# Performance work log

Hardware: AMD Instinct MI355X
Metric: run time of the kernel (lower is better)

## Reference

```python
import jax, jax.numpy as jnp
import numpy as np

N, F, H, K, E = 10000, 128, 128, 500, 320000
EPS = 1e-15


def setup_inputs() -> dict:
    key = jax.random.key(0)
    ks = jax.random.split(key, 16)
    def lin(k, fi, fo):
        return jax.random.normal(k, (fi, fo), jnp.float32) / np.sqrt(fi).astype(np.float32)
    inp = {
        'nodes': jax.random.normal(ks[0], (N, F), jnp.float32),
        'edges': jax.random.randint(ks[1], (2, E), 0, N, jnp.int32),
        'batch': jnp.zeros((N,), jnp.int32),
        'W1': lin(ks[2], F, H), 'b1': jnp.zeros((H,), jnp.float32),
        'W2': lin(ks[3], H, H), 'b2': jnp.zeros((H,), jnp.float32),
        'pool_W': lin(ks[4], H, K), 'pool_b': jnp.zeros((K,), jnp.float32),
        'W3': lin(ks[5], H, H), 'b3': jnp.zeros((H,), jnp.float32),
        'W4': lin(ks[6], H, H), 'b4': jnp.zeros((H,), jnp.float32),
        'W5': lin(ks[7], H, F), 'b5': jnp.zeros((F,), jnp.float32),
    }
    return inp


def reference(nodes, edges, batch, W1, b1, W2, b2, pool_W, pool_b, W3, b3, W4, b4, W5, b5):
    n = nodes.shape[0]
    row, col = edges[0], edges[1]
    # GCN normalization with self-loops (computed once, shared by all convs)
    loop = jnp.arange(n, dtype=row.dtype)
    row_sl = jnp.concatenate([row, loop])
    col_sl = jnp.concatenate([col, loop])
    deg = jax.ops.segment_sum(jnp.ones_like(col_sl, dtype=nodes.dtype), col_sl, num_segments=n)
    dinv = jnp.where(deg > 0, 1.0 / jnp.sqrt(deg), 0.0)
    norm = dinv[row_sl] * dinv[col_sl]  # [E+N]

    def gcn(x, W, b):
        h = x @ W
        msg = h[row_sl] * norm[:, None]
        return jax.ops.segment_sum(msg, col_sl, num_segments=n) + b

    x = jnp.tanh(gcn(nodes, W1, b1))
    x = jnp.tanh(gcn(x, W2, b2))

    # dense batch (single graph) + dense adjacency [1, N, N]
    adj = jnp.zeros((n, n), x.dtype).at[row, col].add(1.0)[None]
    xd = x[None]                                   # [1, N, H]
    s_logits = xd @ pool_W + pool_b                # [1, N, K]

    # ---- dense_mincut_pool ----
    s = jax.nn.softmax(s_logits, axis=-1)
    k = s.shape[-1]
    out = jnp.einsum('bnk,bnh->bkh', s, xd)        # s^T x, [1, K, H]
    a_s = adj @ s                                  # [1, N, K]
    out_adj = jnp.swapaxes(s, 1, 2) @ a_s          # s^T A s, [1, K, K]
    mincut_num = jnp.trace(out_adj, axis1=1, axis2=2)
    d_flat = adj.sum(-1)                           # [1, N]
    # trace(s^T D s) = sum_n d_n * sum_k s_nk^2
    mincut_den = jnp.einsum('bn,bnk,bnk->b', d_flat, s, s) + EPS
    mincut_loss = jnp.mean(-(mincut_num / mincut_den))
    ss = jnp.swapaxes(s, 1, 2) @ s                 # [1, K, K]
    ss_norm = jnp.linalg.norm(ss, axis=(-1, -2), keepdims=True)
    i_s_normed = jnp.eye(k, dtype=ss.dtype) / jnp.sqrt(jnp.asarray(k, ss.dtype))
    ortho_loss = jnp.mean(jnp.linalg.norm(ss / (ss_norm + EPS) - i_s_normed, axis=(-1, -2)))
    # zero diagonal, then symmetric degree normalization
    out_adj = out_adj * (1.0 - jnp.eye(k, dtype=out_adj.dtype))
    d = jnp.sqrt(out_adj.sum(-1))[:, None] + EPS   # [1, 1, K]
    out_adj = out_adj / d / jnp.swapaxes(d, 1, 2)
    # ---- end pool ----

    s2 = jax.nn.softmax(s_logits, axis=-1)
    x_out = (s2 @ out)[0]                          # [N, H]
    adj_out = s2 @ (out_adj @ jnp.swapaxes(s2, 1, 2))  # [1, N, N]

    # recon_adj = False -> reuse original edge_index
    x = jnp.tanh(gcn(x_out, W3, b3))
    x = jnp.tanh(gcn(x, W4, b4))
    x = gcn(x, W5, b5)
    return x, adj_out, mincut_loss, ortho_loss
```

## Files before the change

### kernel.cpp

```cpp
#include <hip/hip_runtime.h>
#include <hip/hip_bf16.h>
#include <math.h>

#define EPSF 1e-15f

typedef __attribute__((ext_vector_type(8))) short bf16x8;
typedef __attribute__((ext_vector_type(4))) float f32x4;

__device__ __forceinline__ void gload_lds16(const void* g, void* l){
  __builtin_amdgcn_global_load_lds(
    (const __attribute__((address_space(1))) unsigned int*)(g),
    (__attribute__((address_space(3))) unsigned int*)(l), 16, 0, 0);
}


__global__ void k_count_deg(const int* __restrict__ edges, int E, int* indeg, int* outdeg){
  int e = blockIdx.x*blockDim.x + threadIdx.x;
  if (e >= E) return;
  int r = edges[e], c = edges[E+e];
  atomicAdd(&outdeg[r], 1);
  atomicAdd(&indeg[c], 1);
}

__global__ void k_scan_fused(const int* __restrict__ cnt, int* __restrict__ rowptr,
                             int* __restrict__ cur, float* __restrict__ dinvOut, int n){
  __shared__ int csum[257];
  const int T = 256;
  int chunk = (n + T - 1)/T;
  int t = threadIdx.x;
  int beg = t*chunk, end = min(n, beg + chunk);
  int s = 0;
  for (int i = beg; i < end; ++i) s += cnt[i];
  csum[t+1] = s;
  if (t == 0) csum[0] = 0;
  __syncthreads();
  if (t == 0){ for (int i = 1; i <= T; ++i) csum[i] += csum[i-1]; }
  __syncthreads();
  int acc = csum[t];
  for (int i = beg; i < end; ++i){
    rowptr[i] = acc;
    cur[i] = acc;
    if (dinvOut) dinvOut[i] = rsqrtf((float)(cnt[i] + 1));
    acc += cnt[i];
  }
  if (t == T-1) rowptr[n] = csum[T];
}

__global__ void k_fill_csr(const int* __restrict__ edges, int E, int* cur_in, int* cur_out,
                           int* __restrict__ src, int* __restrict__ dst){
  int e = blockIdx.x*blockDim.x + threadIdx.x;
  if (e >= E) return;
  int r = edges[e], c = edges[E+e];
  int p = atomicAdd(&cur_in[c], 1);  src[p] = r;
  int q = atomicAdd(&cur_out[r], 1); dst[q] = c;
}

__global__ __launch_bounds__(128)
void k_gcn_agg_b(const __hip_bfloat16* __restrict__ hb, const float* __restrict__ dinv,
                 const int* __restrict__ rowptr, const int* __restrict__ src,
                 const float* __restrict__ bias, float* __restrict__ outf,
                 __hip_bfloat16* __restrict__ outb, int Hd, int do_tanh){
  int c = blockIdx.x;
  int t = threadIdx.x;
  float dc = dinv[c];
  float sum = __bfloat162float(hb[(size_t)c*Hd + t]) * dc;
  float sum2 = 0.f;
  int e0 = rowptr[c], e1 = rowptr[c+1];
  int e = e0;
  for (; e + 1 < e1; e += 2){
    int sa = src[e], sb2 = src[e+1];
    sum  += __bfloat162float(hb[(size_t)sa*Hd  + t]) * dinv[sa];
    sum2 += __bfloat162float(hb[(size_t)sb2*Hd + t]) * dinv[sb2];
  }
  if (e < e1){
    int sa = src[e];
    sum += __bfloat162float(hb[(size_t)sa*Hd + t]) * dinv[sa];
  }
  sum += sum2;
  float v = sum * dc + bias[t];
  if (do_tanh) v = tanhf(v);
  if (outf) outf[(size_t)c*Hd + t] = v;
  if (outb) outb[(size_t)c*Hd + t] = __float2bfloat16(v);
}

__global__ __launch_bounds__(256)
void k_as_agg_b2(const __hip_bfloat16* __restrict__ sb, const int* __restrict__ rowptr,
                 const int* __restrict__ dst, float* __restrict__ a_s, int K2, int KP2){
  int n = blockIdx.x;
  int e0 = rowptr[n], e1 = rowptr[n+1];
  const unsigned* sb32 = (const unsigned*)sb;
  for (int k = threadIdx.x; k < K2; k += blockDim.x){
    float a0 = 0.f, a1 = 0.f;
    for (int e = e0; e < e1; ++e){
      unsigned v = sb32[(size_t)dst[e]*KP2 + k];
      a0 += __uint_as_float(v << 16);
      a1 += __uint_as_float(v & 0xFFFF0000u);
    }
    float2* o = (float2*)(a_s + (size_t)n*(K2*2));
    o[k] = make_float2(a0, a1);
  }
}

__global__ void k_pack_bf16pad(const float* __restrict__ x, __hip_bfloat16* __restrict__ y,
                               int rows, int K, int KP){
  long long n = (long long)rows*KP;
  for (long long i = (long long)blockIdx.x*blockDim.x + threadIdx.x; i < n;
       i += (long long)gridDim.x*blockDim.x){
    int row = (int)(i / KP), col = (int)(i - (long long)row*KP);
    y[i] = (col < K) ? __float2bfloat16(x[(size_t)row*K + col]) : __float2bfloat16(0.f);
  }
}

__device__ __forceinline__ void transpose_tile(const float* X, __hip_bfloat16* XT,
                                               int R, int C, int Cp, int Np,
                                               int bx, int by){
  __shared__ float t[32][33];
  int jb = bx*32;
  int ib = by*32;
  int tx = threadIdx.x & 31, ty = threadIdx.x >> 5;
  #pragma unroll
  for (int k = 0; k < 4; ++k){
    int i = ib + ty + k*8, j = jb + tx;
    t[ty + k*8][tx] = (i < R && j < C) ? X[(size_t)i*C + j] : 0.f;
  }
  __syncthreads();
  #pragma unroll
  for (int k = 0; k < 4; ++k){
    int jr = jb + ty + k*8, ic = ib + tx;
    if (jr < Cp && ic < Np)
      XT[(size_t)jr*Np + ic] = __float2bfloat16(t[tx][ty + k*8]);
  }
}

__global__ __launch_bounds__(256)
void k_transpose_f2b(const float* __restrict__ X, __hip_bfloat16* __restrict__ XT,
                     int R, int C, int Cp, int Np){
  transpose_tile(X, XT, R, C, Cp, Np, blockIdx.x, blockIdx.y);
}

struct TPar { const float* src; __hip_bfloat16* dst; int R, C, Cp, Np; };

__global__ __launch_bounds__(256)
void k_transpose_batch6(TPar p0, TPar p1, TPar p2, TPar p3, TPar p4, TPar p5){
  TPar p;
  switch (blockIdx.z){
    case 0: p = p0; break;
    case 1: p = p1; break;
    case 2: p = p2; break;
    case 3: p = p3; break;
    case 4: p = p4; break;
    default: p = p5; break;
  }
  if ((int)blockIdx.x >= (p.Cp + 31)/32 || (int)blockIdx.y >= (p.Np + 31)/32) return;
  transpose_tile(p.src, p.dst, p.R, p.C, p.Cp, p.Np, blockIdx.x, blockIdx.y);
}

__global__ __launch_bounds__(256)
void k_transpose_batch2(const float* __restrict__ X0, __hip_bfloat16* __restrict__ T0,
                        const float* __restrict__ X1, __hip_bfloat16* __restrict__ T1,
                        int R, int C, int Cp, int Np){
  const float* X = blockIdx.z ? X1 : X0;
  __hip_bfloat16* XT = blockIdx.z ? T1 : T0;
  transpose_tile(X, XT, R, C, Cp, Np, blockIdx.x, blockIdx.y);
}

#define MT 128
#define NT 128
#define KT 32
__global__ __launch_bounds__(256)
void k_gemm_abt_mfma(const short* __restrict__ A, const short* __restrict__ B,
                     const float* __restrict__ bias,
                     float* __restrict__ Cf, __hip_bfloat16* __restrict__ Cb,
                     int M, int Nd, int KP, int ldcb, int swz){
  __shared__ __align__(16) short Asl[128*32];
  __shared__ __align__(16) short Bsl[128*32];
  int bx = blockIdx.x, by = blockIdx.y;
  if (swz){
    int gx = gridDim.x;
    int nwg = gx * gridDim.y;
    int bid = by*gx + bx;
    int q = nwg >> 3, r = nwg & 7;
    int xcd = bid & 7, o = bid >> 3;
    int nb = (xcd < r ? xcd*(q+1) : r*(q+1) + (xcd - r)*q) + o;
    bx = nb % gx; by = nb / gx;
  }
  int tid = threadIdx.x;
  int lane = tid & 63, wave = tid >> 6;
  int wr = wave >> 1, wc = wave & 1;
  int l15 = lane & 15, l4 = lane >> 4;
  int tM = by * MT, tN = bx * NT;

  f32x4 acc[4][4];
  #pragma unroll
  for (int i = 0; i < 4; ++i)
    #pragma unroll
    for (int j = 0; j < 4; ++j) acc[i][j] = (f32x4){0.f,0.f,0.f,0.f};

  const short* gA0 = A + (size_t)(tM + (tid>>2))*KP + (tid&3)*8;
  const short* gA1 = A + (size_t)(tM + 64 + (tid>>2))*KP + (tid&3)*8;
  const short* gB0 = B + (size_t)(tN + (tid>>2))*KP + (tid&3)*8;
  const short* gB1 = B + (size_t)(tN + 64 + (tid>>2))*KP + (tid&3)*8;
  short* lA0 = Asl + wave*512;
  short* lA1 = Asl + 2048 + wave*512;
  short* lB0 = Bsl + wave*512;
  short* lB1 = Bsl + 2048 + wave*512;

  for (int k0 = 0; k0 < KP; k0 += KT){
    __syncthreads();
    gload_lds16(gA0 + k0, lA0);
    gload_lds16(gA1 + k0, lA1);
    gload_lds16(gB0 + k0, lB0);
    gload_lds16(gB1 + k0, lB1);
    __syncthreads();

    bf16x8 af[4], bfr[4];
    #pragma unroll
    for (int mi = 0; mi < 4; ++mi)
      af[mi] = *(const bf16x8*)(Asl + (wr*64 + mi*16 + l15)*32 + l4*8);
    #pragma unroll
    for (int nj = 0; nj < 4; ++nj)
      bfr[nj] = *(const bf16x8*)(Bsl + (wc*64 + nj*16 + l15)*32 + l4*8);
    #pragma unroll
    for (int mi = 0; mi < 4; ++mi)
      #pragma unroll
      for (int nj = 0; nj < 4; ++nj)
        acc[mi][nj] = __builtin_amdgcn_mfma_f32_16x16x32_bf16(af[mi], bfr[nj], acc[mi][nj], 0, 0, 0);
  }

  #pragma unroll
  for (int mi = 0; mi < 4; ++mi){
    #pragma unroll
    for (int r = 0; r < 4; ++r){
      int gr = tM + wr*64 + mi*16 + l4*4 + r;
      if (gr >= M) continue;
      #pragma unroll
      for (int nj = 0; nj < 4; ++nj){
        int gc = tN + wc*64 + nj*16 + l15;
        if (gc >= Nd) continue;
        float v = acc[mi][nj][r];
        if (bias) v += bias[gc];
        if (Cf) Cf[(size_t)gr*Nd + gc] = v;
        else    Cb[(size_t)gr*ldcb + gc] = __float2bfloat16(v);
      }
    }
  }
}

__global__ __launch_bounds__(256)
void k_pool_sk(const short* __restrict__ st, const short* __restrict__ xbt,
               const short* __restrict__ a_st,
               float* __restrict__ out_pool, float* __restrict__ P, float* __restrict__ ssm,
               int K, int Hd, int KL, int kChunk){
  __shared__ __align__(16) short Asl[128*32];
  __shared__ __align__(16) short Bsl[128*32];
  int sel = blockIdx.z >> 3;
  int chunk = blockIdx.z & 7;
  const short* B = (sel == 0) ? xbt : (sel == 1) ? a_st : st;
  float* C = (sel == 0) ? out_pool : (sel == 1) ? P : ssm;
  int Nd = (sel == 0) ? Hd : K;
  if ((int)blockIdx.x * NT >= ((sel == 0) ? Hd : 512)) return;
  int tid = threadIdx.x;
  int lane = tid & 63, wave = tid >> 6;
  int wr = wave >> 1, wc = wave & 1;
  int l15 = lane & 15, l4 = lane >> 4;
  int tM = blockIdx.y * MT, tN = blockIdx.x * NT;
  int kBeg = chunk * kChunk;
  int kEnd = min(KL, kBeg + kChunk);

  f32x4 acc[4][4];
  #pragma unroll
  for (int i = 0; i < 4; ++i)
    #pragma unroll
    for (int j = 0; j < 4; ++j) acc[i][j] = (f32x4){0.f,0.f,0.f,0.f};

  const short* gA0 = st + (size_t)(tM + (tid>>2))*KL + (tid&3)*8;
  const short* gA1 = st + (size_t)(tM + 64 + (tid>>2))*KL + (tid&3)*8;
  const short* gB0 = B + (size_t)(tN + (tid>>2))*KL + (tid&3)*8;
  const short* gB1 = B + (size_t)(tN + 64 + (tid>>2))*KL + (tid&3)*8;
  short* lA0 = Asl + wave*512;
  short* lA1 = Asl + 2048 + wave*512;
  short* lB0 = Bsl + wave*512;
  short* lB1 = Bsl + 2048 + wave*512;

  for (int k0 = kBeg; k0 < kEnd; k0 += KT){
    __syncthreads();
    gload_lds16(gA0 + k0, lA0);
    gload_lds16(gA1 + k0, lA1);
    gload_lds16(gB0 + k0, lB0);
    gload_lds16(gB1 + k0, lB1);
    __syncthreads();

    bf16x8 af[4], bfr[4];
    #pragma unroll
    for (int mi = 0; mi < 4; ++mi)
      af[mi] = *(const bf16x8*)(Asl + (wr*64 + mi*16 + l15)*32 + l4*8);
    #pragma unroll
    for (int nj = 0; nj < 4; ++nj)
      bfr[nj] = *(const bf16x8*)(Bsl + (wc*64 + nj*16 + l15)*32 + l4*8);
    #pragma unroll
    for (int mi = 0; mi < 4; ++mi)
      #pragma unroll
      for (int nj = 0; nj < 4; ++nj)
        acc[mi][nj] = __builtin_amdgcn_mfma_f32_16x16x32_bf16(af[mi], bfr[nj], acc[mi][nj], 0, 0, 0);
  }

  #pragma unroll
  for (int mi = 0; mi < 4; ++mi){
    #pragma unroll
    for (int r = 0; r < 4; ++r){
      int gr = tM + wr*64 + mi*16 + l4*4 + r;
      if (gr >= K) continue;
      #pragma unroll
      for (int nj = 0; nj < 4; ++nj){
        int gc = tN + wc*64 + nj*16 + l15;
        if (gc >= Nd) continue;
        atomicAdd(&C[(size_t)gr*Nd + gc], acc[mi][nj][r]);
      }
    }
  }
}


__global__ __launch_bounds__(256)
void k_softmax(float* __restrict__ s, __hip_bfloat16* __restrict__ sb,
               const int* __restrict__ outdeg,
               float* __restrict__ scalars, int N, int K, int KP){
  int wid = threadIdx.x >> 6, lane = threadIdx.x & 63;
  int row = blockIdx.x*4 + wid;
  if (row >= N) return;
  float* sr = s + (size_t)row*K;
  __hip_bfloat16* sbr = sb + (size_t)row*KP;
  float v[8];
  float m = -INFINITY;
  #pragma unroll
  for (int i = 0; i < 8; ++i){
    int k = lane + i*64;
    v[i] = (k < K) ? sr[k] : -INFINITY;
    m = fmaxf(m, v[i]);
  }
  for (int off = 32; off; off >>= 1) m = fmaxf(m, __shfl_xor(m, off));
  float sum = 0.f;
  #pragma unroll
  for (int i = 0; i < 8; ++i){
    int k = lane + i*64;
    if (k < K){ v[i] = expf(v[i] - m); sum += v[i]; } else v[i] = 0.f;
  }
  for (int off = 32; off; off >>= 1) sum += __shfl_xor(sum, off);
  float inv = 1.f / sum;
  float ssq = 0.f;
  #pragma unroll
  for (int i = 0; i < 8; ++i){
    int k = lane + i*64;
    if (k < K){
      float p = v[i]*inv;
      sr[k] = p;
      sbr[k] = __float2bfloat16(p);
      ssq += p*p;
    }
  }
  for (int off = 32; off; off >>= 1) ssq += __shfl_xor(ssq, off);
  if (lane == 0) atomicAdd(&scalars[1], (float)outdeg[row] * ssq);
}

__global__ void k_stats1(const float* __restrict__ P, const float* __restrict__ ssm,
                         float* __restrict__ scalars, int K){
  float tr = 0.f, sq = 0.f;
  int n = K*K;
  for (int idx = blockIdx.x*blockDim.x + threadIdx.x; idx < n; idx += gridDim.x*blockDim.x){
    float v = ssm[idx]; sq += v*v;
    int i = idx / K, j = idx - i*K;
    if (i == j) tr += P[idx];
  }
  for (int off = 32; off; off >>= 1){
    tr += __shfl_xor(tr, off);
    sq += __shfl_xor(sq, off);
  }
  if ((threadIdx.x & 63) == 0){
    if (tr != 0.f) atomicAdd(&scalars[0], tr);
    atomicAdd(&scalars[2], sq);
  }
}

__global__ __launch_bounds__(256)
void k_rowsum_d(const float* __restrict__ P, float* __restrict__ dvec, int K){
  int wid = threadIdx.x >> 6, lane = threadIdx.x & 63;
  int row = blockIdx.x*4 + wid;
  if (row >= K) return;
  const float* pr = P + (size_t)row*K;
  float rs = 0.f;
  for (int j = lane; j < K; j += 64) if (j != row) rs += pr[j];
  for (int off = 32; off; off >>= 1) rs += __shfl_xor(rs, off);
  if (lane == 0) dvec[row] = sqrtf(rs) + EPSF;
}

__global__ void k_stats2(float* __restrict__ P, const float* __restrict__ ssm,
                         const float* __restrict__ dvec,
                         const float* __restrict__ scalars, float* __restrict__ out3, int K){
  float inv = 1.f / (sqrtf(scalars[2]) + EPSF);
  float isk = rsqrtf((float)K);
  float a = 0.f;
  int n = K*K;
  for (int idx = blockIdx.x*blockDim.x + threadIdx.x; idx < n; idx += gridDim.x*blockDim.x){
    int i = idx / K, j = idx - i*K;
    float v = ssm[idx]*inv - ((i == j) ? isk : 0.f);
    a += v*v;
    float pv = P[idx];
    P[idx] = (i == j) ? 0.f : pv / (dvec[i]*dvec[j]);
  }
  for (int off = 32; off; off >>= 1) a += __shfl_xor(a, off);
  if ((threadIdx.x & 63) == 0) atomicAdd(out3, a);
}

__global__ void k_finalize(const float* __restrict__ scalars, float* __restrict__ out2){
  if (threadIdx.x == 0){
    out2[0] = -(scalars[0] / (scalars[1] + EPSF));
    out2[1] = sqrtf(scalars[3]);
  }
}


extern "C" void kernel_launch(void* const* d_in, const int* in_sizes, int n_in,
                              void* d_out, int out_size, void* d_ws, size_t ws_size,
                              hipStream_t stream) {
  const float* nodes = (const float*)d_in[0];
  const int*   edges = (const int*)d_in[1];
  const float* W1 = (const float*)d_in[3];  const float* b1 = (const float*)d_in[4];
  const float* W2 = (const float*)d_in[5];  const float* b2 = (const float*)d_in[6];
  const float* pW = (const float*)d_in[7];  const float* pB = (const float*)d_in[8];
  const float* W3 = (const float*)d_in[9];  const float* b3 = (const float*)d_in[10];
  const float* W4 = (const float*)d_in[11]; const float* b4 = (const float*)d_in[12];
  const float* W5 = (const float*)d_in[13]; const float* b5 = (const float*)d_in[14];

  const int H = 128, F = 128, N = 10000, E = 320000, K = 500;
  const int KP = 512;
  const int NP = 10016;
  const int MP = 79*128;
  (void)n_in; (void)out_size; (void)in_sizes;

  float* out_x   = (float*)d_out;
  float* out_adj = out_x + (size_t)N*F;
  float* out_ls  = out_adj + (size_t)N*N;

  char* ws = (char*)d_ws;
  size_t off = 0;
  auto alloc = [&](size_t bytes) -> void* {
    off = (off + 255) & ~(size_t)255;
    void* p = ws + off;
    off += bytes;
    return p;
  };
  int*   deg2       = (int*)alloc((size_t)2*N*4);
  int*   indeg      = deg2;
  int*   outdeg     = deg2 + N;
  float* zf         = (float*)alloc(((size_t)K*H + 2*(size_t)K*K + 64)*4);
  float* out_pool   = zf;
  float* P          = zf + (size_t)K*H;
  float* ssm        = P + (size_t)K*K;
  float* scalars    = ssm + (size_t)K*K;
  __hip_bfloat16* sub = (__hip_bfloat16*)alloc((size_t)2*MP*KP*2);
  __hip_bfloat16* s_b = sub;
  __hip_bfloat16* u_b = sub + (size_t)MP*KP;
  int*   rowptr_in  = (int*)alloc((size_t)(N+1)*4);
  int*   rowptr_out = (int*)alloc((size_t)(N+1)*4);
  int*   cur_in     = (int*)alloc((size_t)N*4);
  int*   cur_out    = (int*)alloc((size_t)N*4);
  int*   csr_src    = (int*)alloc((size_t)E*4);
  int*   csr_dst    = (int*)alloc((size_t)E*4);
  float* dinv       = (float*)alloc((size_t)N*4);
  __hip_bfloat16* h_b  = (__hip_bfloat16*)alloc((size_t)N*H*2);
  __hip_bfloat16* nodes_b = (__hip_bfloat16*)alloc((size_t)MP*H*2);
  __hip_bfloat16* xa_b = (__hip_bfloat16*)alloc((size_t)MP*H*2);
  __hip_bfloat16* xb_b = (__hip_bfloat16*)alloc((size_t)MP*H*2);
  float* xb         = (float*)alloc((size_t)N*H*4);
  float* s          = (float*)alloc((size_t)N*K*4);
  float* a_s        = (float*)alloc((size_t)N*K*4);
  float* dvec       = (float*)alloc((size_t)K*4);
  __hip_bfloat16* Pt_b = (__hip_bfloat16*)alloc((size_t)KP*KP*2);
  __hip_bfloat16* st_b = (__hip_bfloat16*)alloc((size_t)KP*NP*2);
  __hip_bfloat16* a_st = (__hip_bfloat16*)alloc((size_t)KP*NP*2);
  __hip_bfloat16* xbt  = (__hip_bfloat16*)alloc((size_t)H*NP*2);
  __hip_bfloat16* opT  = (__hip_bfloat16*)alloc((size_t)H*KP*2);
  __hip_bfloat16* W1t  = (__hip_bfloat16*)alloc((size_t)H*F*2);
  __hip_bfloat16* W2t  = (__hip_bfloat16*)alloc((size_t)H*H*2);
  __hip_bfloat16* W3t  = (__hip_bfloat16*)alloc((size_t)H*H*2);
  __hip_bfloat16* W4t  = (__hip_bfloat16*)alloc((size_t)H*H*2);
  __hip_bfloat16* W5t  = (__hip_bfloat16*)alloc((size_t)F*H*2);
  __hip_bfloat16* pWt  = (__hip_bfloat16*)alloc((size_t)KP*H*2);
  (void)ws_size;

  hipMemsetAsync(deg2, 0, (size_t)2*N*4, stream);
  hipMemsetAsync(zf,   0, ((size_t)K*H + 2*(size_t)K*K + 64)*4, stream);
  hipMemsetAsync(sub,  0, (size_t)2*MP*KP*2, stream);

  int eb = (E + 255)/256;
  k_count_deg<<<eb, 256, 0, stream>>>(edges, E, indeg, outdeg);
  k_scan_fused<<<1, 256, 0, stream>>>(indeg,  rowptr_in,  cur_in,  dinv,    N);
  k_scan_fused<<<1, 256, 0, stream>>>(outdeg, rowptr_out, cur_out, nullptr, N);
  k_fill_csr<<<eb, 256, 0, stream>>>(edges, E, cur_in, cur_out, csr_src, csr_dst);

  {
    TPar p0 = { W1, W1t, F, H, H, F };
    TPar p1 = { W2, W2t, H, H, H, H };
    TPar p2 = { W3, W3t, H, H, H, H };
    TPar p3 = { W4, W4t, H, H, H, H };
    TPar p4 = { W5, W5t, H, F, F, H };
    TPar p5 = { pW, pWt, H, K, KP, H };
    dim3 g(16, 4, 6);
    k_transpose_batch6<<<g, 256, 0, stream>>>(p0, p1, p2, p3, p4, p5);
  }
  k_pack_bf16pad<<<1024, 256, 0, stream>>>(nodes, nodes_b, N, F, F);

  auto mfma = [&](const __hip_bfloat16* A, const __hip_bfloat16* B, const float* bias,
                  float* Cf, __hip_bfloat16* Cb, int M, int Nd, int Kp, int ldcb, int swz){
    dim3 g((Nd + NT - 1)/NT, (M + MT - 1)/MT);
    k_gemm_abt_mfma<<<g, 256, 0, stream>>>((const short*)A, (const short*)B, bias,
                                           Cf, Cb, M, Nd, Kp, ldcb, swz);
  };

  mfma(nodes_b, W1t, nullptr, nullptr, h_b, N, H, F, H, 0);
  k_gcn_agg_b<<<N, H, 0, stream>>>(h_b, dinv, rowptr_in, csr_src, b1, nullptr, xa_b, H, 1);
  mfma(xa_b, W2t, nullptr, nullptr, h_b, N, H, H, H, 0);
  k_gcn_agg_b<<<N, H, 0, stream>>>(h_b, dinv, rowptr_in, csr_src, b2, xb, xb_b, H, 1);

  mfma(xb_b, pWt, pB, s, nullptr, N, K, H, 0, 0);
  k_softmax<<<(N+3)/4, 256, 0, stream>>>(s, s_b, outdeg, scalars, N, K, KP);
  k_as_agg_b2<<<N, 256, 0, stream>>>(s_b, rowptr_out, csr_dst, a_s, K/2, KP/2);
  { dim3 g(KP/32, NP/32, 2); k_transpose_batch2<<<g, 256, 0, stream>>>(s, st_b, a_s, a_st, N, K, KP, NP); }
  { dim3 g(H/32, NP/32); k_transpose_f2b<<<g, 256, 0, stream>>>(xb, xbt, N, H, H, NP); }

  const int kChunk = 1280;
  { dim3 g(4, 4, 24); k_pool_sk<<<g, 256, 0, stream>>>((const short*)st_b, (const short*)xbt,
                                                       (const short*)a_st,
                                                       out_pool, P, ssm, K, H, NP, kChunk); }
  k_stats1<<<128, 256, 0, stream>>>(P, ssm, scalars, K);
  k_rowsum_d<<<(K+3)/4, 256, 0, stream>>>(P, dvec, K);
  k_stats2<<<128, 256, 0, stream>>>(P, ssm, dvec, scalars, &scalars[3], K);
  k_finalize<<<1, 64, 0, stream>>>(scalars, out_ls);

  { dim3 g(KP/32, KP/32); k_transpose_f2b<<<g, 256, 0, stream>>>(P, Pt_b, K, K, KP, KP); }
  mfma(s_b, Pt_b, nullptr, nullptr, u_b, N, K, KP, KP, 0);
  mfma(u_b, s_b, nullptr, out_adj, nullptr, N, N, KP, 0, 1);
  { dim3 g(H/32, KP/32); k_transpose_f2b<<<g, 256, 0, stream>>>(out_pool, opT, K, H, H, KP); }
  mfma(s_b, opT, nullptr, nullptr, xa_b, N, H, KP, H, 0);

  mfma(xa_b, W3t, nullptr, nullptr, h_b, N, H, H, H, 0);
  k_gcn_agg_b<<<N, H, 0, stream>>>(h_b, dinv, rowptr_in, csr_src, b3, nullptr, xb_b, H, 1);
  mfma(xb_b, W4t, nullptr, nullptr, h_b, N, H, H, H, 0);
  k_gcn_agg_b<<<N, H, 0, stream>>>(h_b, dinv, rowptr_in, csr_src, b4, nullptr, xa_b, H, 1);
  mfma(xa_b, W5t, nullptr, nullptr, h_b, N, F, H, F, 0);
  k_gcn_agg_b<<<N, F, 0, stream>>>(h_b, dinv, rowptr_in, csr_src, b5, out_x, nullptr, F, 0);
}
```

Baseline: 900.3 us.

## Vectorize GCN and A·s aggregation, batch transposes and scans, trim memsets

The GCN aggregation now has each 64-lane wave handle one node and read two bf16 values per lane, so a block covers two nodes. The A·s aggregation loads four bf16 values per thread instead of two. The two scans are merged into one launch, the transposes are batched into fewer launches, and the fp32 xb buffer is dropped by transposing directly from bf16. A full memset of the padded s/u buffers is replaced with a kernel that zeroes only the pad regions. Together these reduce launch count, memory traffic and per-thread instruction overhead in the bandwidth-bound scatter kernels.

```diff
diff --git a/kernel.cpp b/kernel.cpp
--- a/kernel.cpp
+++ b/kernel.cpp
@@ -11,6 +11,13 @@
   __builtin_amdgcn_global_load_lds(
     (const __attribute__((address_space(1))) unsigned int*)(g),
     (__attribute__((address_space(3))) unsigned int*)(l), 16, 0, 0);
+}
+
+__device__ __forceinline__ float blo(unsigned v){ return __uint_as_float(v << 16); }
+__device__ __forceinline__ float bhi(unsigned v){ return __uint_as_float(v & 0xFFFF0000u); }
+__device__ __forceinline__ unsigned short b16(float v){
+  __hip_bfloat16 b = __float2bfloat16(v);
+  return *reinterpret_cast<unsigned short*>(&b);
 }
 
 
@@ -22,8 +29,8 @@
   atomicAdd(&indeg[c], 1);
 }
 
-__global__ void k_scan_fused(const int* __restrict__ cnt, int* __restrict__ rowptr,
-                             int* __restrict__ cur, float* __restrict__ dinvOut, int n){
+__device__ __forceinline__ void scan_body(const int* cnt, int* rowptr, int* cur,
+                                          float* dinvOut, int n){
   __shared__ int csum[257];
   const int T = 256;
   int chunk = (n + T - 1)/T;
@@ -46,6 +53,13 @@
   if (t == T-1) rowptr[n] = csum[T];
 }
 
+__global__ void k_scan_batch(const int* __restrict__ indeg, const int* __restrict__ outdeg,
+                             int* rp_in, int* rp_out, int* cur_in, int* cur_out,
+                             float* dinv, int n){
+  if (blockIdx.x == 0) scan_body(indeg,  rp_in,  cur_in,  dinv,    n);
+  else                 scan_body(outdeg, rp_out, cur_out, nullptr, n);
+}
+
 __global__ void k_fill_csr(const int* __restrict__ edges, int E, int* cur_in, int* cur_out,
                            int* __restrict__ src, int* __restrict__ dst){
   int e = blockIdx.x*blockDim.x + threadIdx.x;
@@ -56,48 +70,63 @@
 }
 
 __global__ __launch_bounds__(128)
-void k_gcn_agg_b(const __hip_bfloat16* __restrict__ hb, const float* __restrict__ dinv,
+void k_gcn_agg_v(const __hip_bfloat16* __restrict__ hb, const float* __restrict__ dinv,
                  const int* __restrict__ rowptr, const int* __restrict__ src,
                  const float* __restrict__ bias, float* __restrict__ outf,
-                 __hip_bfloat16* __restrict__ outb, int Hd, int do_tanh){
-  int c = blockIdx.x;
-  int t = threadIdx.x;
+                 __hip_bfloat16* __restrict__ outb, int Hd2, int N, int do_tanh){
+  int c = blockIdx.x*2 + (threadIdx.x >> 6);
+  if (c >= N) return;
+  int lane = threadIdx.x & 63;
+  const unsigned* h32 = (const unsigned*)hb;
   float dc = dinv[c];
-  float sum = __bfloat162float(hb[(size_t)c*Hd + t]) * dc;
-  float sum2 = 0.f;
+  unsigned vs = h32[(size_t)c*Hd2 + lane];
+  float s0 = blo(vs)*dc, s1 = bhi(vs)*dc;
+  float t0 = 0.f, t1 = 0.f;
   int e0 = rowptr[c], e1 = rowptr[c+1];
   int e = e0;
   for (; e + 1 < e1; e += 2){
-    int sa = src[e], sb2 = src[e+1];
-    sum  += __bfloat162float(hb[(size_t)sa*Hd  + t]) * dinv[sa];
-    sum2 += __bfloat162float(hb[(size_t)sb2*Hd + t]) * dinv[sb2];
+    int sa = src[e], sb = src[e+1];
+    float da = dinv[sa], db = dinv[sb];
+    unsigned va = h32[(size_t)sa*Hd2 + lane];
+    unsigned vb = h32[(size_t)sb*Hd2 + lane];
+    s0 += blo(va)*da; s1 += bhi(va)*da;
+    t0 += blo(vb)*db; t1 += bhi(vb)*db;
   }
   if (e < e1){
     int sa = src[e];
-    sum += __bfloat162float(hb[(size_t)sa*Hd + t]) * dinv[sa];
-  }
-  sum += sum2;
-  float v = sum * dc + bias[t];
-  if (do_tanh) v = tanhf(v);
-  if (outf) outf[(size_t)c*Hd + t] = v;
-  if (outb) outb[(size_t)c*Hd + t] = __float2bfloat16(v);
-}
-
-__global__ __launch_bounds__(256)
-void k_as_agg_b2(const __hip_bfloat16* __restrict__ sb, const int* __restrict__ rowptr,
-                 const int* __restrict__ dst, float* __restrict__ a_s, int K2, int KP2){
+    float da = dinv[sa];
+    unsigned va = h32[(size_t)sa*Hd2 + lane];
+    s0 += blo(va)*da; s1 += bhi(va)*da;
+  }
+  s0 += t0; s1 += t1;
+  float2 bb = ((const float2*)bias)[lane];
+  float v0 = s0*dc + bb.x;
+  float v1 = s1*dc + bb.y;
+  if (do_tanh){ v0 = tanhf(v0); v1 = tanhf(v1); }
+  if (outf){
+    ((float2*)(outf + (size_t)c*(Hd2*2)))[lane] = make_float2(v0, v1);
+  }
+  if (outb){
+    unsigned r = ((unsigned)b16(v1) << 16) | (unsigned)b16(v0);
+    ((unsigned*)(outb + (size_t)c*(Hd2*2)))[lane] = r;
+  }
+}
+
+__global__ __launch_bounds__(128)
+void k_as_agg_b4(const __hip_bfloat16* __restrict__ sb, const int* __restrict__ rowptr,
+                 const int* __restrict__ dst, float* __restrict__ a_s,
+                 int K, int K4, int KP4){
   int n = blockIdx.x;
   int e0 = rowptr[n], e1 = rowptr[n+1];
-  const unsigned* sb32 = (const unsigned*)sb;
-  for (int k = threadIdx.x; k < K2; k += blockDim.x){
-    float a0 = 0.f, a1 = 0.f;
+  const uint2* sb64 = (const uint2*)sb;
+  for (int k = threadIdx.x; k < K4; k += blockDim.x){
+    float a0 = 0.f, a1 = 0.f, a2 = 0.f, a3 = 0.f;
     for (int e = e0; e < e1; ++e){
-      unsigned v = sb32[(size_t)dst[e]*KP2 + k];
-      a0 += __uint_as_float(v << 16);
-      a1 += __uint_as_float(v & 0xFFFF0000u);
+      uint2 v = sb64[(size_t)dst[e]*KP4 + k];
+      a0 += blo(v.x); a1 += bhi(v.x);
+      a2 += blo(v.y); a3 += bhi(v.y);
     }
-    float2* o = (float2*)(a_s + (size_t)n*(K2*2));
-    o[k] = make_float2(a0, a1);
+    ((f32x4*)(a_s + (size_t)n*K))[k] = (f32x4){a0, a1, a2, a3};
   }
 }
 
@@ -111,6 +140,26 @@
   }
 }
 
+__global__ void k_zero_pads(__hip_bfloat16* __restrict__ s_b, __hip_bfloat16* __restrict__ u_b,
+                            int N, int K, int KP, int MP){
+  int padc = KP - K;
+  long long nA = (long long)N*padc;
+  long long nB = (long long)(MP - N)*KP;
+  long long tot = 2*(nA + nB);
+  __hip_bfloat16 z = __float2bfloat16(0.f);
+  for (long long i = (long long)blockIdx.x*blockDim.x + threadIdx.x; i < tot;
+       i += (long long)gridDim.x*blockDim.x){
+    long long j = i >> 1;
+    __hip_bfloat16* buf = (i & 1) ? u_b : s_b;
+    if (j < nA){
+      int row = (int)(j / padc), col = K + (int)(j % padc);
+      buf[(size_t)row*KP + col] = z;
+    } else {
+      buf[(size_t)N*KP + (j - nA)] = z;
+    }
+  }
+}
+
 __device__ __forceinline__ void transpose_tile(const float* X, __hip_bfloat16* XT,
                                                int R, int C, int Cp, int Np,
                                                int bx, int by){
@@ -132,10 +181,25 @@
   }
 }
 
-__global__ __launch_bounds__(256)
-void k_transpose_f2b(const float* __restrict__ X, __hip_bfloat16* __restrict__ XT,
-                     int R, int C, int Cp, int Np){
-  transpose_tile(X, XT, R, C, Cp, Np, blockIdx.x, blockIdx.y);
+__device__ __forceinline__ void transpose_tile_b(const __hip_bfloat16* X, __hip_bfloat16* XT,
+                                                 int R, int C, int Cp, int Np,
+                                                 int bx, int by){
+  __shared__ float tb[32][33];
+  int jb = bx*32;
+  int ib = by*32;
+  int tx = threadIdx.x & 31, ty = threadIdx.x >> 5;
+  #pragma unroll
+  for (int k = 0; k < 4; ++k){
+    int i = ib + ty + k*8, j = jb + tx;
+    tb[ty + k*8][tx] = (i < R && j < C) ? __bfloat162float(X[(size_t)i*C + j]) : 0.f;
+  }
+  __syncthreads();
+  #pragma unroll
+  for (int k = 0; k < 4; ++k){
+    int jr = jb + ty + k*8, ic = ib + tx;
+    if (jr < Cp && ic < Np)
+      XT[(size_t)jr*Np + ic] = __float2bfloat16(tb[tx][ty + k*8]);
+  }
 }
 
 struct TPar { const float* src; __hip_bfloat16* dst; int R, C, Cp, Np; };
@@ -156,12 +220,29 @@
 }
 
 __global__ __launch_bounds__(256)
-void k_transpose_batch2(const float* __restrict__ X0, __hip_bfloat16* __restrict__ T0,
-                        const float* __restrict__ X1, __hip_bfloat16* __restrict__ T1,
-                        int R, int C, int Cp, int Np){
-  const float* X = blockIdx.z ? X1 : X0;
-  __hip_bfloat16* XT = blockIdx.z ? T1 : T0;
-  transpose_tile(X, XT, R, C, Cp, Np, blockIdx.x, blockIdx.y);
+void k_transpose_batch3(const float* __restrict__ s, __hip_bfloat16* __restrict__ st,
+                        const float* __restrict__ a_s, __hip_bfloat16* __restrict__ a_st,
+                        const __hip_bfloat16* __restrict__ xbb, __hip_bfloat16* __restrict__ xbt,
+                        int N, int K, int KP, int Hd, int NP){
+  int z = blockIdx.z;
+  if (z < 2){
+    transpose_tile(z ? a_s : s, z ? a_st : st, N, K, KP, NP, blockIdx.x, blockIdx.y);
+  } else {
+    if ((int)blockIdx.x*32 >= Hd) return;
+    transpose_tile_b(xbb, xbt, N, Hd, Hd, NP, blockIdx.x, blockIdx.y);
+  }
+}
+
+__global__ __launch_bounds__(256)
+void k_transpose_ptop(const float* __restrict__ P, __hip_bfloat16* __restrict__ Pt,
+                      const float* __restrict__ op, __hip_bfloat16* __restrict__ opT,
+                      int K, int KP, int Hd){
+  if (blockIdx.z == 0){
+    transpose_tile(P, Pt, K, K, KP, KP, blockIdx.x, blockIdx.y);
+  } else {
+    if ((int)blockIdx.x*32 >= Hd) return;
+    transpose_tile(op, opT, K, Hd, Hd, KP, blockIdx.x, blockIdx.y);
+  }
 }
 
 #define MT 128
@@ -457,9 +538,8 @@
   float* P          = zf + (size_t)K*H;
   float* ssm        = P + (size_t)K*K;
   float* scalars    = ssm + (size_t)K*K;
-  __hip_bfloat16* sub = (__hip_bfloat16*)alloc((size_t)2*MP*KP*2);
-  __hip_bfloat16* s_b = sub;
-  __hip_bfloat16* u_b = sub + (size_t)MP*KP;
+  __hip_bfloat16* s_b = (__hip_bfloat16*)alloc((size_t)MP*KP*2);
+  __hip_bfloat16* u_b = (__hip_bfloat16*)alloc((size_t)MP*KP*2);
   int*   rowptr_in  = (int*)alloc((size_t)(N+1)*4);
   int*   rowptr_out = (int*)alloc((size_t)(N+1)*4);
   int*   cur_in     = (int*)alloc((size_t)N*4);
@@ -467,11 +547,10 @@
   int*   csr_src    = (int*)alloc((size_t)E*4);
   int*   csr_dst    = (int*)alloc((size_t)E*4);
   float* dinv       = (float*)alloc((size_t)N*4);
-  __hip_bfloat16* h_b  = (__hip_bfloat16*)alloc((size_t)N*H*2);
+  __hip_bfloat16* h_b  = (__hip_bfloat16*)alloc((size_t)N*H*2 + 32768);
   __hip_bfloat16* nodes_b = (__hip_bfloat16*)alloc((size_t)MP*H*2);
   __hip_bfloat16* xa_b = (__hip_bfloat16*)alloc((size_t)MP*H*2);
   __hip_bfloat16* xb_b = (__hip_bfloat16*)alloc((size_t)MP*H*2);
-  float* xb         = (float*)alloc((size_t)N*H*4);
   float* s          = (float*)alloc((size_t)N*K*4);
   float* a_s        = (float*)alloc((size_t)N*K*4);
   float* dvec       = (float*)alloc((size_t)K*4);
@@ -490,12 +569,12 @@
 
   hipMemsetAsync(deg2, 0, (size_t)2*N*4, stream);
   hipMemsetAsync(zf,   0, ((size_t)K*H + 2*(size_t)K*K + 64)*4, stream);
-  hipMemsetAsync(sub,  0, (size_t)2*MP*KP*2, stream);
+  k_zero_pads<<<512, 256, 0, stream>>>(s_b, u_b, N, K, KP, MP);
 
   int eb = (E + 255)/256;
   k_count_deg<<<eb, 256, 0, stream>>>(edges, E, indeg, outdeg);
-  k_scan_fused<<<1, 256, 0, stream>>>(indeg,  rowptr_in,  cur_in,  dinv,    N);
-  k_scan_fused<<<1, 256, 0, stream>>>(outdeg, rowptr_out, cur_out, nullptr, N);
+  k_scan_batch<<<2, 256, 0, stream>>>(indeg, outdeg, rowptr_in, rowptr_out,
+                                      cur_in, cur_out, dinv, N);
   k_fill_csr<<<eb, 256, 0, stream>>>(edges, E, cur_in, cur_out, csr_src, csr_dst);
 
   {
@@ -518,16 +597,15 @@
   };
 
   mfma(nodes_b, W1t, nullptr, nullptr, h_b, N, H, F, H, 0);
-  k_gcn_agg_b<<<N, H, 0, stream>>>(h_b, dinv, rowptr_in, csr_src, b1, nullptr, xa_b, H, 1);
+  k_gcn_agg_v<<<N/2, 128, 0, stream>>>(h_b, dinv, rowptr_in, csr_src, b1, nullptr, xa_b, H/2, N, 1);
   mfma(xa_b, W2t, nullptr, nullptr, h_b, N, H, H, H, 0);
-  k_gcn_agg_b<<<N, H, 0, stream>>>(h_b, dinv, rowptr_in, csr_src, b2, xb, xb_b, H, 1);
+  k_gcn_agg_v<<<N/2, 128, 0, stream>>>(h_b, dinv, rowptr_in, csr_src, b2, nullptr, xb_b, H/2, N, 1);
 
   mfma(xb_b, pWt, pB, s, nullptr, N, K, H, 0, 0);
   k_softmax<<<(N+3)/4, 256, 0, stream>>>(s, s_b, outdeg, scalars, N, K, KP);
-  k_as_agg_b2<<<N, 256, 0, stream>>>(s_b, rowptr_out, csr_dst, a_s, K/2, KP/2);
-  { dim3 g(KP/32, NP/32, 2); k_transpose_batch2<<<g, 256, 0, stream>>>(s, st_b, a_s, a_st, N, K, KP, NP); }
-  { dim3 g(H/32, NP/32); k_transpose_f2b<<<g, 256, 0, stream>>>(xb, xbt, N, H, H, NP); }
-
+  k_as_agg_b4<<<N, 128, 0, stream>>>(s_b, rowptr_out, csr_dst, a_s, K, K/4, KP/4);
+  { dim3 g(KP/32, NP/32, 3); k_transpose_batch3<<<g, 256, 0, stream>>>(s, st_b, a_s, a_st,
+                                                                       xb_b, xbt, N, K, KP, H, NP); }
   const int kChunk = 1280;
   { dim3 g(4, 4, 24); k_pool_sk<<<g, 256, 0, stream>>>((const short*)st_b, (const short*)xbt,
                                                        (const short*)a_st,
@@ -537,16 +615,15 @@
   k_stats2<<<128, 256, 0, stream>>>(P, ssm, dvec, scalars, &scalars[3], K);
   k_finalize<<<1, 64, 0, stream>>>(scalars, out_ls);
 
-  { dim3 g(KP/32, KP/32); k_transpose_f2b<<<g, 256, 0, stream>>>(P, Pt_b, K, K, KP, KP); }
+  { dim3 g(16, 16, 2); k_transpose_ptop<<<g, 256, 0, stream>>>(P, Pt_b, out_pool, opT, K, KP, H); }
   mfma(s_b, Pt_b, nullptr, nullptr, u_b, N, K, KP, KP, 0);
   mfma(u_b, s_b, nullptr, out_adj, nullptr, N, N, KP, 0, 1);
-  { dim3 g(H/32, KP/32); k_transpose_f2b<<<g, 256, 0, stream>>>(out_pool, opT, K, H, H, KP); }
   mfma(s_b, opT, nullptr, nullptr, xa_b, N, H, KP, H, 0);
 
   mfma(xa_b, W3t, nullptr, nullptr, h_b, N, H, H, H, 0);
-  k_gcn_agg_b<<<N, H, 0, stream>>>(h_b, dinv, rowptr_in, csr_src, b3, nullptr, xb_b, H, 1);
+  k_gcn_agg_v<<<N/2, 128, 0, stream>>>(h_b, dinv, rowptr_in, csr_src, b3, nullptr, xb_b, H/2, N, 1);
   mfma(xb_b, W4t, nullptr, nullptr, h_b, N, H, H, H, 0);
-  k_gcn_agg_b<<<N, H, 0, stream>>>(h_b, dinv, rowptr_in, csr_src, b4, nullptr, xa_b, H, 1);
+  k_gcn_agg_v<<<N/2, 128, 0, stream>>>(h_b, dinv, rowptr_in, csr_src, b4, nullptr, xa_b, H/2, N, 1);
   mfma(xa_b, W5t, nullptr, nullptr, h_b, N, F, H, F, 0);
-  k_gcn_agg_b<<<N, F, 0, stream>>>(h_b, dinv, rowptr_in, csr_src, b5, out_x, nullptr, F, 0);
-}
+  k_gcn_agg_v<<<N/2, 128, 0, stream>>>(h_b, dinv, rowptr_in, csr_src, b5, out_x, nullptr, F/2, N, 0);
+}
```

Result: faster. 833.8 us (-7.4%).
